# Optimization experiments

Measured on AMD Instinct MI355X. Metric: run time of the kernel, lower is better.

## Reference

```python
import jax, jax.numpy as jnp
import numpy as np

N_DIMS = 1024
N_HEADS = 16
HEAD_DIM = N_DIMS // N_HEADS


def setup_inputs() -> dict:
    key = jax.random.key(0)
    k_x, k_wa, k_wp = jax.random.split(key, 3)
    x = jax.random.normal(k_x, (4, 2048, N_DIMS), dtype=jnp.float32)
    # nn.Linear weights stored [out, in]; apply as x @ W.T
    scale_a = 1.0 / np.sqrt(N_DIMS)
    w_attn = jax.random.uniform(k_wa, (3 * N_DIMS, N_DIMS), jnp.float32, -scale_a, scale_a)
    w_proj = jax.random.uniform(k_wp, (N_DIMS, N_DIMS), jnp.float32, -scale_a, scale_a)
    return {"x": x, "w_attn": w_attn, "w_proj": w_proj}


def reference(x, w_attn, w_proj):
    B, S, D = x.shape
    qkv = x @ w_attn.T                                  # [B, S, 3D]
    q, k, v = jnp.split(qkv, 3, axis=-1)
    # [B, H, S, Dh]
    def heads(t):
        return t.reshape(B, S, N_HEADS, HEAD_DIM).transpose(0, 2, 1, 3)
    q, k, v = heads(q), heads(k), heads(v)
    scores = jnp.einsum('bhqd,bhkd->bhqk', q, k) * (1.0 / np.sqrt(HEAD_DIM))
    causal = jnp.tril(jnp.ones((S, S), dtype=bool))
    scores = jnp.where(causal[None, None], scores, -jnp.inf)
    attn = jax.nn.softmax(scores, axis=-1)              # dropout: eval mode (identity)
    y = jnp.einsum('bhqk,bhkd->bhqd', attn, v)
    y = y.transpose(0, 2, 1, 3).reshape(B, S, D)
    return y @ w_proj.T
```

## Files before the change

kernel.cpp:

```cpp
#include <hip/hip_runtime.h>

typedef unsigned short ushort_t;
typedef __attribute__((ext_vector_type(8))) short bf16x8;
typedef __attribute__((ext_vector_type(4))) float f32x4;


__device__ __forceinline__ ushort_t f2bf(float f) {
    union { float f; unsigned u; } c; c.f = f;
    unsigned u = c.u;
    unsigned r = (u + 0x7fffu + ((u >> 16) & 1u)) >> 16;
    return (ushort_t)r;
}

__device__ __forceinline__ unsigned fbits(float f) {
    union { float f; unsigned u; } c; c.f = f; return c.u;
}

__device__ __forceinline__ void gld_lds16(const ushort_t* g, ushort_t* l) {
    __builtin_amdgcn_global_load_lds(
        (const __attribute__((address_space(1))) void*)g,
        (__attribute__((address_space(3))) void*)l, 16, 0, 0);
}


__global__ void convert_bf16(const float* __restrict__ in, ushort_t* __restrict__ out, int n4) {
    int i = blockIdx.x * blockDim.x + threadIdx.x;
    if (i < n4) {
        const float4 f = ((const float4*)in)[i];
        ushort4 o;
        o.x = f2bf(f.x); o.y = f2bf(f.y); o.z = f2bf(f.z); o.w = f2bf(f.w);
        ((ushort4*)out)[i] = o;
    }
}


__global__ __launch_bounds__(256) void gemm_qkv(
    const ushort_t* __restrict__ A, const ushort_t* __restrict__ W,
    ushort_t* __restrict__ qo, ushort_t* __restrict__ ko, ushort_t* __restrict__ vto)
{
    constexpr int K = 1024;
    const int m0 = blockIdx.x * 128;
    const int n0 = blockIdx.y * 128;
    __shared__ alignas(16) ushort_t smem[8192];
    ushort_t* sA = smem;
    ushort_t* sB = smem + 4096;
    const int tid = threadIdx.x;
    const int wave = tid >> 6, lane = tid & 63;
    const int quad = lane >> 4, l16 = lane & 15;
    const int wm = (wave >> 1) << 6, wn = (wave & 1) << 6;
    const int srow = lane >> 2;
    const int scol = (((lane & 3) ^ ((srow >> 1) & 3)) << 3);
    const int fg = ((quad ^ ((l16 >> 1) & 3)) << 3);

    f32x4 acc[4][4] = {};
    const ushort_t* aRow0 = A + (size_t)(m0 + wave * 32 + srow) * K + scol;
    const ushort_t* bRow0 = W + (size_t)(n0 + wave * 32 + srow) * K + scol;

    for (int k0 = 0; k0 < K; k0 += 32) {
#pragma unroll
        for (int c = 0; c < 2; ++c) {
            gld_lds16(aRow0 + (size_t)c * 16 * K + k0, sA + (wave * 2 + c) * 512);
            gld_lds16(bRow0 + (size_t)c * 16 * K + k0, sB + (wave * 2 + c) * 512);
        }
        __syncthreads();
        bf16x8 af[4], bfr[4];
#pragma unroll
        for (int f = 0; f < 4; ++f) {
            af[f]  = *(const bf16x8*)(sA + (wm + f * 16 + l16) * 32 + fg);
            bfr[f] = *(const bf16x8*)(sB + (wn + f * 16 + l16) * 32 + fg);
        }
#pragma unroll
        for (int mf = 0; mf < 4; ++mf)
#pragma unroll
            for (int nf = 0; nf < 4; ++nf)
                acc[mf][nf] = __builtin_amdgcn_mfma_f32_16x16x32_bf16(af[mf], bfr[nf], acc[mf][nf], 0, 0, 0);
        __syncthreads();
    }

    const int which = n0 >> 10;
    ushort_t* sT = smem + wave * 2048;
    const int b  = (m0 + wm) >> 11;
    const int sb = (m0 + wm) & 2047;
    const int h  = ((n0 + wn) & 1023) >> 6;
    const int bh = b * 16 + h;

    if (which < 2) {
        ushort_t* go = (which == 0) ? qo : ko;
        const float qs1 = (which == 0) ? 0.18033688011112042f : 1.0f;
#pragma unroll
        for (int mf = 0; mf < 4; ++mf) {
#pragma unroll
            for (int nf = 0; nf < 4; ++nf)
#pragma unroll
                for (int i = 0; i < 4; ++i) {
                    const int mll = quad * 4 + i;
                    sT[mll * 64 + ((nf * 16 + l16) ^ (4 * (mll & 7)))] = f2bf(acc[mf][nf][i] * qs1);
                }
            __builtin_amdgcn_s_waitcnt(0);
#pragma unroll
            for (int p = 0; p < 4; ++p) {
                const int mll = p * 4 + quad;
                const ushort4 val = *(const ushort4*)(sT + mll * 64 + ((l16 * 4) ^ (4 * (mll & 7))));
                const int s = sb + mf * 16 + mll;
                *(ushort4*)(go + ((size_t)bh * 2048 + s) * 64 + l16 * 4) = val;
            }
            __builtin_amdgcn_s_waitcnt(0);
        }
    } else {
#pragma unroll
        for (int nf = 0; nf < 4; ++nf) {
#pragma unroll
            for (int mf = 0; mf < 4; ++mf) {
                ushort4 w;
                w.x = f2bf(acc[mf][nf][0]);
                w.y = f2bf(acc[mf][nf][1]);
                w.z = f2bf(acc[mf][nf][2]);
                w.w = f2bf(acc[mf][nf][3]);
                *(ushort4*)(sT + l16 * 64 + ((mf * 16 + quad * 4) ^ (4 * (l16 & 7)))) = w;
            }
            __builtin_amdgcn_s_waitcnt(0);
#pragma unroll
            for (int p = 0; p < 4; ++p) {
                const int nll = p * 4 + quad;
                const ushort4 val = *(const ushort4*)(sT + nll * 64 + ((l16 * 4) ^ (4 * (nll & 7))));
                const int dh = nf * 16 + nll;
                *(ushort4*)(vto + ((size_t)bh * 64 + dh) * 2048 + sb + l16 * 4) = val;
            }
            __builtin_amdgcn_s_waitcnt(0);
        }
    }
}


__global__ __launch_bounds__(256) void attn(
    const ushort_t* __restrict__ qg_, const ushort_t* __restrict__ kg_,
    const ushort_t* __restrict__ vg_, ushort_t* __restrict__ y)
{
    const int bh = blockIdx.x;
    const int b = bh >> 4, h = bh & 15;
    const int tid = threadIdx.x, wave = tid >> 6, lane = tid & 63;
    const int quad = lane >> 4, l16 = lane & 15;
    const int l8 = lane & 7;

    __shared__ alignas(16) ushort_t sQP[128 * 64];
    __shared__ alignas(16) ushort_t sK[64 * 64];
    __shared__ alignas(16) ushort_t sV[64 * 64];

    const ushort_t* kg = kg_ + (size_t)bh * 2048 * 64;
    const ushort_t* vg = vg_ + (size_t)bh * 64 * 2048;

    const int srow8 = lane >> 3;
    const int sg = ((l8 ^ srow8) << 3);
    ushort_t* sPw = sQP + wave * 2048;

    for (int pass = 0; pass < 2; ++pass) {
        const int qy = pass ? (15 - (int)blockIdx.y) : (int)blockIdx.y;
        const int q0 = qy * 128;
        const ushort_t* qg = qg_ + ((size_t)bh * 2048 + q0) * 64;

        __syncthreads();
        {
            const int row = lane >> 3, e = l8 << 3;
#pragma unroll
            for (int c = 0; c < 4; ++c) {
                const int chunk = wave * 4 + c;
                gld_lds16(qg + (size_t)(chunk * 8 + row) * 64 + e, sQP + chunk * 512);
            }
        }
        __syncthreads();

        bf16x8 bq[2][2];
#pragma unroll
        for (int qf = 0; qf < 2; ++qf)
#pragma unroll
            for (int ks = 0; ks < 2; ++ks)
                bq[qf][ks] = *(const bf16x8*)(sQP + (wave * 32 + qf * 16 + l16) * 64 + ks * 32 + quad * 8);

        f32x4 oacc[2][4] = {};
        float lpart[2] = {0.f, 0.f};

        const int ktiles = 2 * qy + 2;
        const int wrmin = q0 + wave * 32, wrmax = wrmin + 31;

        for (int t = 0; t < ktiles; ++t) {
            const int k0 = t * 64;
            __syncthreads();
#pragma unroll
            for (int c = 0; c < 2; ++c) {
                const int chunk = wave * 2 + c;
                gld_lds16(kg + (size_t)(k0 + chunk * 8 + srow8) * 64 + sg, sK + chunk * 512);
                gld_lds16(vg + (size_t)(chunk * 8 + srow8) * 2048 + k0 + sg, sV + chunk * 512);
            }
            __syncthreads();
            if (k0 > wrmax) continue;

            f32x4 sacc[4][2] = {};
#pragma unroll
            for (int ks = 0; ks < 2; ++ks) {
                bf16x8 ak[4];
#pragma unroll
                for (int kf = 0; kf < 4; ++kf)
                    ak[kf] = *(const bf16x8*)(sK + (kf * 16 + l16) * 64 + (((ks * 4 + quad) ^ l8) << 3));
#pragma unroll
                for (int kf = 0; kf < 4; ++kf)
#pragma unroll
                    for (int qf = 0; qf < 2; ++qf)
                        sacc[kf][qf] = __builtin_amdgcn_mfma_f32_16x16x32_bf16(ak[kf], bq[qf][ks], sacc[kf][qf], 0, 0, 0);
            }

            const bool diag = (k0 + 63 > wrmin);
#pragma unroll
            for (int kf = 0; kf < 4; ++kf) {
#pragma unroll
                for (int qf = 0; qf < 2; ++qf) {
                    float p[4];
#pragma unroll
                    for (int i = 0; i < 4; ++i) {
                        float sv = sacc[kf][qf][i];
                        if (diag) {
                            const int cg = k0 + kf * 16 + quad * 4 + i;
                            const int rg = wrmin + qf * 16 + l16;
                            sv = (cg <= rg) ? sv : -3.0e38f;
                        }
                        p[i] = __builtin_amdgcn_exp2f(sv);
                        lpart[qf] += p[i];
                    }
                    uint2 w;
                    w.x = ((fbits(p[0]) + 0x8000u) >> 16) | ((fbits(p[1]) + 0x8000u) & 0xffff0000u);
                    w.y = ((fbits(p[2]) + 0x8000u) >> 16) | ((fbits(p[3]) + 0x8000u) & 0xffff0000u);
                    *(uint2*)(sPw + (qf * 16 + l16) * 64 +
                              (((kf * 2 + (quad >> 1)) ^ l8) << 3) + ((quad & 1) << 2)) = w;
                }
            }

#pragma unroll
            for (int ks = 0; ks < 2; ++ks) {
                bf16x8 pa[2], vb[4];
                const int rgrp = (((ks * 4 + quad) ^ l8) << 3);
#pragma unroll
                for (int mf = 0; mf < 2; ++mf)
                    pa[mf] = *(const bf16x8*)(sPw + (mf * 16 + l16) * 64 + rgrp);
#pragma unroll
                for (int nf = 0; nf < 4; ++nf)
                    vb[nf] = *(const bf16x8*)(sV + (nf * 16 + l16) * 64 + rgrp);
#pragma unroll
                for (int mf = 0; mf < 2; ++mf)
#pragma unroll
                    for (int nf = 0; nf < 4; ++nf)
                        oacc[mf][nf] = __builtin_amdgcn_mfma_f32_16x16x32_bf16(pa[mf], vb[nf], oacc[mf][nf], 0, 0, 0);
            }
        }

        float rl[2];
#pragma unroll
        for (int qf = 0; qf < 2; ++qf) {
            float x = lpart[qf];
            x += __shfl_xor(x, 16);
            x += __shfl_xor(x, 32);
            rl[qf] = x;
        }
#pragma unroll
        for (int mf = 0; mf < 2; ++mf) {
#pragma unroll
            for (int i = 0; i < 4; ++i) {
                const float inv = 1.0f / __shfl(rl[mf], quad * 4 + i);
                const int r = q0 + wave * 32 + mf * 16 + quad * 4 + i;
#pragma unroll
                for (int nf = 0; nf < 4; ++nf)
                    y[((size_t)b * 2048 + r) * 1024 + h * 64 + nf * 16 + l16] =
                        f2bf(oacc[mf][nf][i] * inv);
            }
        }
    }
}


__global__ __launch_bounds__(256) void gemm_proj(
    const ushort_t* __restrict__ A, const ushort_t* __restrict__ W, float* __restrict__ out)
{
    constexpr int K = 1024;
    const int m0 = blockIdx.x * 128;
    const int n0 = blockIdx.y * 128;
    __shared__ alignas(16) ushort_t sA[128 * 32];
    __shared__ alignas(16) ushort_t sB[128 * 32];
    const int tid = threadIdx.x;
    const int wave = tid >> 6, lane = tid & 63;
    const int quad = lane >> 4, l16 = lane & 15;
    const int wm = (wave >> 1) << 6, wn = (wave & 1) << 6;
    const int srow = lane >> 2;
    const int scol = (((lane & 3) ^ ((srow >> 1) & 3)) << 3);
    const int fg = ((quad ^ ((l16 >> 1) & 3)) << 3);

    f32x4 acc[4][4] = {};
    const ushort_t* aRow0 = A + (size_t)(m0 + wave * 32 + srow) * K + scol;
    const ushort_t* bRow0 = W + (size_t)(n0 + wave * 32 + srow) * K + scol;

    for (int k0 = 0; k0 < K; k0 += 32) {
#pragma unroll
        for (int c = 0; c < 2; ++c) {
            gld_lds16(aRow0 + (size_t)c * 16 * K + k0, sA + (wave * 2 + c) * 512);
            gld_lds16(bRow0 + (size_t)c * 16 * K + k0, sB + (wave * 2 + c) * 512);
        }
        __syncthreads();
        bf16x8 af[4], bfr[4];
#pragma unroll
        for (int f = 0; f < 4; ++f) {
            af[f]  = *(const bf16x8*)(sA + (wm + f * 16 + l16) * 32 + fg);
            bfr[f] = *(const bf16x8*)(sB + (wn + f * 16 + l16) * 32 + fg);
        }
#pragma unroll
        for (int mf = 0; mf < 4; ++mf)
#pragma unroll
            for (int nf = 0; nf < 4; ++nf)
                acc[mf][nf] = __builtin_amdgcn_mfma_f32_16x16x32_bf16(af[mf], bfr[nf], acc[mf][nf], 0, 0, 0);
        __syncthreads();
    }

#pragma unroll
    for (int mf = 0; mf < 4; ++mf)
#pragma unroll
        for (int nf = 0; nf < 4; ++nf)
#pragma unroll
            for (int i = 0; i < 4; ++i) {
                const int m = m0 + wm + mf * 16 + quad * 4 + i;
                const int n = n0 + wn + nf * 16 + l16;
                out[(size_t)m * 1024 + n] = acc[mf][nf][i];
            }
}


extern "C" void kernel_launch(void* const* d_in, const int* in_sizes, int n_in,
                              void* d_out, int out_size, void* d_ws, size_t ws_size,
                              hipStream_t stream) {
    const float* x  = (const float*)d_in[0];
    const float* wa = (const float*)d_in[1];
    const float* wp = (const float*)d_in[2];
    float* out = (float*)d_out;

    char* ws = (char*)d_ws;
    ushort_t* xb  = (ushort_t*)(ws);
    ushort_t* wab = (ushort_t*)(ws + 16777216);
    ushort_t* wpb = (ushort_t*)(ws + 16777216 + 6291456);
    ushort_t* q   = (ushort_t*)(ws + 25165824);
    ushort_t* k   = (ushort_t*)(ws + 41943040);
    ushort_t* vt  = (ushort_t*)(ws + 58720256);
    ushort_t* y   = xb;

    convert_bf16<<<8192 * 1024 / 4 / 256, 256, 0, stream>>>(x, xb, 8192 * 1024 / 4);
    convert_bf16<<<3072 * 1024 / 4 / 256, 256, 0, stream>>>(wa, wab, 3072 * 1024 / 4);
    convert_bf16<<<1024 * 1024 / 4 / 256, 256, 0, stream>>>(wp, wpb, 1024 * 1024 / 4);

    gemm_qkv<<<dim3(64, 24), 256, 0, stream>>>(xb, wab, q, k, vt);
    attn<<<dim3(64, 8), 256, 0, stream>>>(q, k, vt, y);
    gemm_proj<<<dim3(64, 8), 256, 0, stream>>>(y, wpb, out);
}
```

Before: 257.5 us.

## Shrink attention query tile to 64 rows and double the grid

The attention kernel now handles 64 query rows per block (16 per wave) instead of 128, and the grid grows from 8 to 16 blocks in y, still with two causal-balanced passes per block. The aim is more blocks for occupancy and less wasted masked work on diagonal tiles, plus a smaller LDS footprint. The cost is that each K/V tile loaded into LDS now feeds half as many MFMAs, so global and LDS traffic per unit of compute rise. P is now written to LDS one scalar bf16 at a time instead of as packed uint2 stores, and the Q load waits on a waitcnt rather than a barrier.

```diff
diff --git a/kernel.cpp b/kernel.cpp
--- a/kernel.cpp
+++ b/kernel.cpp
@@ -12,8 +12,9 @@
     return (ushort_t)r;
 }
 
-__device__ __forceinline__ unsigned fbits(float f) {
-    union { float f; unsigned u; } c; c.f = f; return c.u;
+__device__ __forceinline__ ushort_t f2bf_fast(float f) {
+    union { float f; unsigned u; } c; c.f = f;
+    return (ushort_t)((c.u + 0x8000u) >> 16);
 }
 
 __device__ __forceinline__ void gld_lds16(const ushort_t* g, ushort_t* l) {
@@ -142,47 +143,41 @@
     const int quad = lane >> 4, l16 = lane & 15;
     const int l8 = lane & 7;
 
-    __shared__ alignas(16) ushort_t sQP[128 * 64];
-    __shared__ alignas(16) ushort_t sK[64 * 64];
-    __shared__ alignas(16) ushort_t sV[64 * 64];
+    __shared__ alignas(16) ushort_t sQP[4096];
+    __shared__ alignas(16) ushort_t sK[4096];
+    __shared__ alignas(16) ushort_t sV[4096];
 
     const ushort_t* kg = kg_ + (size_t)bh * 2048 * 64;
     const ushort_t* vg = vg_ + (size_t)bh * 64 * 2048;
 
     const int srow8 = lane >> 3;
     const int sg = ((l8 ^ srow8) << 3);
-    ushort_t* sPw = sQP + wave * 2048;
+    ushort_t* sPw = sQP + wave * 1024;
 
     for (int pass = 0; pass < 2; ++pass) {
-        const int qy = pass ? (15 - (int)blockIdx.y) : (int)blockIdx.y;
-        const int q0 = qy * 128;
-        const ushort_t* qg = qg_ + ((size_t)bh * 2048 + q0) * 64;
+        const int qy = pass ? (31 - (int)blockIdx.y) : (int)blockIdx.y;
+        const int q0 = qy * 64;
 
         __syncthreads();
         {
-            const int row = lane >> 3, e = l8 << 3;
-#pragma unroll
-            for (int c = 0; c < 4; ++c) {
-                const int chunk = wave * 4 + c;
-                gld_lds16(qg + (size_t)(chunk * 8 + row) * 64 + e, sQP + chunk * 512);
-            }
-        }
-        __syncthreads();
-
-        bf16x8 bq[2][2];
-#pragma unroll
-        for (int qf = 0; qf < 2; ++qf)
-#pragma unroll
-            for (int ks = 0; ks < 2; ++ks)
-                bq[qf][ks] = *(const bf16x8*)(sQP + (wave * 32 + qf * 16 + l16) * 64 + ks * 32 + quad * 8);
-
-        f32x4 oacc[2][4] = {};
-        float lpart[2] = {0.f, 0.f};
-
-        const int ktiles = 2 * qy + 2;
-        const int wrmin = q0 + wave * 32, wrmax = wrmin + 31;
-
-        for (int t = 0; t < ktiles; ++t) {
+            const ushort_t* qg = qg_ + ((size_t)bh * 2048 + q0 + wave * 16) * 64;
+#pragma unroll
+            for (int c = 0; c < 2; ++c)
+                gld_lds16(qg + (size_t)(c * 8 + srow8) * 64 + sg, sQP + (wave * 2 + c) * 512);
+        }
+        __builtin_amdgcn_s_waitcnt(0);
+
+        bf16x8 bq[2];
+#pragma unroll
+        for (int ks = 0; ks < 2; ++ks)
+            bq[ks] = *(const bf16x8*)(sQP + (wave * 16 + l16) * 64 + (((ks * 4 + quad) ^ l8) << 3));
+
+        f32x4 oacc[4] = {};
+        float lpart = 0.f;
+
+        const int wrow = q0 + wave * 16 + l16;
+
+        for (int t = 0; t <= qy; ++t) {
             const int k0 = t * 64;
             __syncthreads();
 #pragma unroll
@@ -192,9 +187,8 @@
                 gld_lds16(vg + (size_t)(chunk * 8 + srow8) * 2048 + k0 + sg, sV + chunk * 512);
             }
             __syncthreads();
-            if (k0 > wrmax) continue;
-
-            f32x4 sacc[4][2] = {};
+
+            f32x4 sacc[4] = {};
 #pragma unroll
             for (int ks = 0; ks < 2; ++ks) {
                 bf16x8 ak[4];
@@ -203,73 +197,50 @@
                     ak[kf] = *(const bf16x8*)(sK + (kf * 16 + l16) * 64 + (((ks * 4 + quad) ^ l8) << 3));
 #pragma unroll
                 for (int kf = 0; kf < 4; ++kf)
-#pragma unroll
-                    for (int qf = 0; qf < 2; ++qf)
-                        sacc[kf][qf] = __builtin_amdgcn_mfma_f32_16x16x32_bf16(ak[kf], bq[qf][ks], sacc[kf][qf], 0, 0, 0);
-            }
-
-            const bool diag = (k0 + 63 > wrmin);
-#pragma unroll
-            for (int kf = 0; kf < 4; ++kf) {
-#pragma unroll
-                for (int qf = 0; qf < 2; ++qf) {
-                    float p[4];
-#pragma unroll
-                    for (int i = 0; i < 4; ++i) {
-                        float sv = sacc[kf][qf][i];
-                        if (diag) {
-                            const int cg = k0 + kf * 16 + quad * 4 + i;
-                            const int rg = wrmin + qf * 16 + l16;
-                            sv = (cg <= rg) ? sv : -3.0e38f;
-                        }
-                        p[i] = __builtin_amdgcn_exp2f(sv);
-                        lpart[qf] += p[i];
+                    sacc[kf] = __builtin_amdgcn_mfma_f32_16x16x32_bf16(ak[kf], bq[ks], sacc[kf], 0, 0, 0);
+            }
+
+            const bool diag = (t == qy);
+#pragma unroll
+            for (int kf = 0; kf < 4; ++kf)
+#pragma unroll
+                for (int i = 0; i < 4; ++i) {
+                    float sv = sacc[kf][i];
+                    if (diag) {
+                        const int cg = k0 + kf * 16 + quad * 4 + i;
+                        sv = (cg <= wrow) ? sv : -3.0e38f;
                     }
-                    uint2 w;
-                    w.x = ((fbits(p[0]) + 0x8000u) >> 16) | ((fbits(p[1]) + 0x8000u) & 0xffff0000u);
-                    w.y = ((fbits(p[2]) + 0x8000u) >> 16) | ((fbits(p[3]) + 0x8000u) & 0xffff0000u);
-                    *(uint2*)(sPw + (qf * 16 + l16) * 64 +
-                              (((kf * 2 + (quad >> 1)) ^ l8) << 3) + ((quad & 1) << 2)) = w;
+                    const float p = __builtin_amdgcn_exp2f(sv);
+                    lpart += p;
+                    const int c = kf * 16 + quad * 4 + i;
+                    sPw[l16 * 64 + (((c >> 3) ^ l8) << 3) + (c & 7)] = f2bf_fast(p);
                 }
-            }
 
 #pragma unroll
             for (int ks = 0; ks < 2; ++ks) {
-                bf16x8 pa[2], vb[4];
                 const int rgrp = (((ks * 4 + quad) ^ l8) << 3);
-#pragma unroll
-                for (int mf = 0; mf < 2; ++mf)
-                    pa[mf] = *(const bf16x8*)(sPw + (mf * 16 + l16) * 64 + rgrp);
+                const bf16x8 pa = *(const bf16x8*)(sPw + l16 * 64 + rgrp);
+                bf16x8 vb[4];
 #pragma unroll
                 for (int nf = 0; nf < 4; ++nf)
                     vb[nf] = *(const bf16x8*)(sV + (nf * 16 + l16) * 64 + rgrp);
 #pragma unroll
-                for (int mf = 0; mf < 2; ++mf)
-#pragma unroll
-                    for (int nf = 0; nf < 4; ++nf)
-                        oacc[mf][nf] = __builtin_amdgcn_mfma_f32_16x16x32_bf16(pa[mf], vb[nf], oacc[mf][nf], 0, 0, 0);
-            }
-        }
-
-        float rl[2];
-#pragma unroll
-        for (int qf = 0; qf < 2; ++qf) {
-            float x = lpart[qf];
-            x += __shfl_xor(x, 16);
-            x += __shfl_xor(x, 32);
-            rl[qf] = x;
-        }
-#pragma unroll
-        for (int mf = 0; mf < 2; ++mf) {
-#pragma unroll
-            for (int i = 0; i < 4; ++i) {
-                const float inv = 1.0f / __shfl(rl[mf], quad * 4 + i);
-                const int r = q0 + wave * 32 + mf * 16 + quad * 4 + i;
-#pragma unroll
                 for (int nf = 0; nf < 4; ++nf)
-                    y[((size_t)b * 2048 + r) * 1024 + h * 64 + nf * 16 + l16] =
-                        f2bf(oacc[mf][nf][i] * inv);
-            }
+                    oacc[nf] = __builtin_amdgcn_mfma_f32_16x16x32_bf16(pa, vb[nf], oacc[nf], 0, 0, 0);
+            }
+        }
+
+        float rs = lpart;
+        rs += __shfl_xor(rs, 16);
+        rs += __shfl_xor(rs, 32);
+#pragma unroll
+        for (int i = 0; i < 4; ++i) {
+            const float inv = 1.0f / __shfl(rs, quad * 4 + i);
+            const int r = q0 + wave * 16 + quad * 4 + i;
+#pragma unroll
+            for (int nf = 0; nf < 4; ++nf)
+                y[((size_t)b * 2048 + r) * 1024 + h * 64 + nf * 16 + l16] =
+                    f2bf(oacc[nf][i] * inv);
         }
     }
 }
@@ -351,6 +322,6 @@
     convert_bf16<<<1024 * 1024 / 4 / 256, 256, 0, stream>>>(wp, wpb, 1024 * 1024 / 4);
 
     gemm_qkv<<<dim3(64, 24), 256, 0, stream>>>(xb, wab, q, k, vt);
-    attn<<<dim3(64, 8), 256, 0, stream>>>(q, k, vt, y);
+    attn<<<dim3(64, 16), 256, 0, stream>>>(q, k, vt, y);
     gemm_proj<<<dim3(64, 8), 256, 0, stream>>>(y, wpb, out);
 }
```

New measurement: 253.1 us. Within noise of the previous version (-1.7%).
